# Kernel optimization log

Hardware: AMD Instinct MI355X
Metric: run time of the kernel (lower is better)

Reference implementation:

```python
import jax, jax.numpy as jnp
import numpy as np

B, L, S, V = 1024, 512, 64, 160000
EMB = 16
E = 3 * EMB            # extended embedding dim = 48
G, M = 4, 3            # lsh_group_num, lsh_group_length
MAXC = 2 ** M          # 8 buckets per group
NH, KD = 8, 4          # MHA heads / key_dim
IN_DIM = 5 * EMB + 3 * E   # user(80) + item(48) + longterm(48) + shortterm(48) = 224
PAD_LT, PAD_ST = L // 4, S // 4
M_VALUES = jnp.array([1, 2, 4], dtype=jnp.float32)
LN_EPS = 1e-3  # keras LayerNormalization default


def setup_inputs() -> dict:
    key = jax.random.key(0)
    ks = list(jax.random.split(key, 40))
    d = {}
    for i, n in enumerate(['uid', 'utag1', 'utag2', 'utag3', 'utag4']):
        d[n] = jax.random.randint(ks[i], (B,), 1, V, dtype=jnp.int32)
    for i, n in enumerate(['label_goods_ids', 'label_shop_ids', 'label_cate_ids']):
        d[n] = jax.random.randint(ks[5 + i], (B,), 1, V, dtype=jnp.int32)
    for i, n in enumerate(['longterm_goods_ids', 'longterm_shop_ids', 'longterm_cate_ids']):
        ids = jax.random.randint(ks[8 + i], (B, L), 1, V, dtype=jnp.int32)
        d[n] = ids.at[:, L - PAD_LT:].set(0)  # left-aligned valid prefix, padded tail
    for i, n in enumerate(['shortterm_goods_ids', 'shortterm_shop_ids', 'shortterm_cate_ids']):
        ids = jax.random.randint(ks[11 + i], (B, S), 1, V, dtype=jnp.int32)
        d[n] = ids.at[:, S - PAD_ST:].set(0)
    def nrm(k, shape, s):
        return jax.random.normal(k, shape, jnp.float32) * s
    d['embed_table'] = nrm(ks[14], (V, EMB), 0.05)
    d['H'] = nrm(ks[15], (E, G, M), 1.0)  # non-trainable LSH projections
    d['wq'] = nrm(ks[16], (E, NH, KD), 0.1); d['bq'] = jnp.zeros((NH, KD))
    d['wk'] = nrm(ks[17], (E, NH, KD), 0.1); d['bk'] = jnp.zeros((NH, KD))
    d['wv'] = nrm(ks[18], (E, NH, KD), 0.1); d['bv'] = jnp.zeros((NH, KD))
    d['wo'] = nrm(ks[19], (NH, KD, E), 0.1); d['bo'] = jnp.zeros((E,))
    d['w1'] = nrm(ks[20], (IN_DIM, 200), 0.1); d['b1'] = jnp.zeros((200,))
    d['g1'] = jnp.ones((200,)); d['be1'] = jnp.zeros((200,))
    d['w2'] = nrm(ks[21], (200, 80), 0.1); d['b2'] = jnp.zeros((80,))
    d['g2'] = jnp.ones((80,)); d['be2'] = jnp.zeros((80,))
    d['w3'] = nrm(ks[22], (80, 1), 0.1); d['b3'] = jnp.zeros((1,))
    return d


def _stack_embed(table, feats):
    # feats: list of (B,) or (B,T) int arrays -> (B, T, n_feats*EMB)
    cols = [f[:, None] if f.ndim == 1 else f for f in feats]
    X = jnp.stack(cols, axis=2)              # (B, T, F)
    Xe = table[X]                            # (B, T, F, EMB)
    return Xe.reshape(Xe.shape[0], Xe.shape[1], -1)


def _layernorm(x, g, b):
    mu = x.mean(-1, keepdims=True)
    var = jnp.square(x - mu).mean(-1, keepdims=True)
    return g * (x - mu) / jnp.sqrt(var + LN_EPS) + b


def _lsh_codes(x, H):
    # x: (B, T, E) -> integer bucket codes (B, T, G)
    codes = jnp.sign(jnp.einsum('bte,egm->btgm', x, H))
    binary = (codes == 1).astype(jnp.float32)
    return jnp.tensordot(binary, M_VALUES, axes=[[-1], [0]]).astype(jnp.int32)


def _forward(uid, utag1, utag2, utag3, utag4,
             label_goods_ids, label_shop_ids, label_cate_ids,
             longterm_goods_ids, longterm_shop_ids, longterm_cate_ids,
             shortterm_goods_ids, shortterm_shop_ids, shortterm_cate_ids,
             embed_table, H, wq, bq, wk, bk, wv, bv, wo, bo,
             w1, b1, g1, be1, w2, b2, g2, be2, w3, b3):
    # --- embeddings ---
    Xu = _stack_embed(embed_table, [uid, utag1, utag2, utag3, utag4])        # (B,1,80)
    Xi = _stack_embed(embed_table, [label_goods_ids, label_shop_ids, label_cate_ids])  # (B,1,48)
    Xl = _stack_embed(embed_table, [longterm_goods_ids, longterm_shop_ids, longterm_cate_ids])   # (B,L,48)
    Xs = _stack_embed(embed_table, [shortterm_goods_ids, shortterm_shop_ids, shortterm_cate_ids])  # (B,S,48)

    longterm_pad = longterm_goods_ids == 0
    shortterm_pad = shortterm_goods_ids == 0

    # --- long-term interest: LSH scatter-mean over buckets then gather by item code ---
    series_int = _lsh_codes(Xl, H)                                   # (B,L,G)
    mXl = Xl * (~longterm_pad).astype(jnp.float32)[:, :, None]        # masked series embeddings
    oh = jax.nn.one_hot(series_int, MAXC, dtype=jnp.float32)          # (B,L,G,C)
    c_sum = jnp.einsum('blgc,ble->bgce', oh, mXl)                     # bucket sums (B,G,C,E)
    vc = oh.sum(axis=1)                                               # valid counts (B,G,C)
    safe = jnp.where(vc[..., None] > 0,
                     c_sum / jnp.maximum(vc[..., None], 1.0),
                     0.0)                                             # bucket means
    item_int = _lsh_codes(Xi, H)                                      # (B,1,G)
    item_oh = jax.nn.one_hot(item_int, MAXC, dtype=jnp.float32)       # (B,1,G,C)
    longterm_interest = jnp.einsum('bgce,bsgc->bsge', safe, item_oh).mean(axis=2)  # (B,1,E)

    # --- short-term interest: target attention (keras MultiHeadAttention) ---
    lengths = (~shortterm_pad).astype(jnp.int32).sum(axis=1)           # (B,)
    seq_mask = (jnp.arange(S)[None, :] < lengths[:, None]).astype(jnp.float32)  # (B,S)
    q = jnp.einsum('bqe,ehd->bqhd', Xi, wq) + bq
    k = jnp.einsum('bke,ehd->bkhd', Xs, wk) + bk
    v = jnp.einsum('bke,ehd->bkhd', Xs, wv) + bv
    scores = jnp.einsum('bqhd,bkhd->bhqk', q, k) / jnp.sqrt(jnp.float32(KD))
    scores = scores + (1.0 - seq_mask[:, None, None, :]) * (-1e9)
    attn = jax.nn.softmax(scores, axis=-1)
    ctx = jnp.einsum('bhqk,bkhd->bqhd', attn, v)
    shortterm_interest = jnp.einsum('bqhd,hde->bqe', ctx, wo) + bo      # (B,1,E)

    # --- final MLP: Dense->LN->ReLU x2, Dense->sigmoid ---
    feat = jnp.concatenate([Xu[:, 0], Xi[:, 0],
                            longterm_interest[:, 0], shortterm_interest[:, 0]], axis=-1)  # (B,224)
    h = jax.nn.relu(_layernorm(feat @ w1 + b1, g1, be1))
    h = jax.nn.relu(_layernorm(h @ w2 + b2, g2, be2))
    return jax.nn.sigmoid(h @ w3 + b3)                                 # (B,1)


def reference(uid, utag1, utag2, utag3, utag4,
              label_goods_ids, label_shop_ids, label_cate_ids,
              longterm_goods_ids, longterm_shop_ids, longterm_cate_ids,
              shortterm_goods_ids, shortterm_shop_ids, shortterm_cate_ids,
              embed_table, H, wq, bq, wk, bk, wv, bv, wo, bo,
              w1, b1, g1, be1, w2, b2, g2, be2, w3, b3):
    return _forward(uid, utag1, utag2, utag3, utag4,
                    label_goods_ids, label_shop_ids, label_cate_ids,
                    longterm_goods_ids, longterm_shop_ids, longterm_cate_ids,
                    shortterm_goods_ids, shortterm_shop_ids, shortterm_cate_ids,
                    embed_table, H, wq, bq, wk, bk, wv, bv, wo, bo,
                    w1, b1, g1, be1, w2, b2, g2, be2, w3, b3)
```

## Files before the change

kernel.cpp:

```cpp
#include <hip/hip_runtime.h>
#include <hip/hip_bf16.h>

#define LLEN 512
#define SLEN 64
#define EMBD 16
#define EE 48
#define GG 4
#define NHH 8
#define KDD 4
#define INDIM 224
#define H1D 200
#define H2D 80
#define CHUNK 128
#define PXE 52
#define NT 512

__device__ __forceinline__ float bf2f(unsigned short u) {
    union { unsigned int i; float f; } v; v.i = ((unsigned int)u) << 16; return v.f;
}

template<bool BF16>
__device__ __forceinline__ float ldf(const void* p, int i) {
    if constexpr (BF16) return bf2f(((const unsigned short*)p)[i]);
    else                return ((const float*)p)[i];
}

template<bool BF16>
__device__ __forceinline__ float4 ld4(const void* p, int i4) {
    if constexpr (BF16) {
        ushort4 u = ((const ushort4*)p)[i4 >> 2];
        return make_float4(bf2f(u.x), bf2f(u.y), bf2f(u.z), bf2f(u.w));
    } else {
        return ((const float4*)p)[i4 >> 2];
    }
}

struct Pool {
    float buf[CHUNK * PXE + 16];
    float part[8][GG][EE];
    float hf[12 * EE];
    float feat[INDIM];
    float q[NHH * KDD];
    float red[128];
    int   pcw[8][2];
    int   icode[GG];
    int   len;
    float mu, rstd;
};

template<bool BF16>
__device__ void sdim_body(Pool& P,
    const int* uid, const int* ut1, const int* ut2, const int* ut3, const int* ut4,
    const int* lb_g, const int* lb_s, const int* lb_c,
    const int* lt_g, const int* lt_s, const int* lt_c,
    const int* st_g, const int* st_s, const int* st_c,
    const void* tbl, const void* Hm,
    const void* wq, const void* bq, const void* wk, const void* bk,
    const void* wvv, const void* bv, const void* wo, const void* bo,
    const void* w1, const void* b1, const void* g1, const void* be1,
    const void* w2, const void* b2, const void* g2, const void* be2,
    const void* w3, const void* b3, void* outp)
{
    const int b = blockIdx.x;
    const int tid = threadIdx.x;
    const int lane = tid & 63;
    const int wid = __builtin_amdgcn_readfirstlane(tid >> 6);

    for (int i = tid; i < 12 * EE; i += NT) {
        int j = i / EE, e = i - j * EE;
        P.hf[i] = ldf<BF16>(Hm, e * 12 + j);
    }
    if (tid < 80) {
        int f = tid >> 4, e = tid & 15;
        int id = (f == 0) ? uid[b] : (f == 1) ? ut1[b] : (f == 2) ? ut2[b] : (f == 3) ? ut3[b] : ut4[b];
        P.feat[tid] = ldf<BF16>(tbl, id * EMBD + e);
    } else if (tid < 128) {
        int t = tid - 80; int f = t >> 4, e = t & 15;
        int id = (f == 0) ? lb_g[b] : (f == 1) ? lb_s[b] : lb_c[b];
        P.feat[80 + t] = ldf<BF16>(tbl, id * EMBD + e);
    }
    __syncthreads();

    if (tid < 32) {
        float acc = ldf<BF16>(bq, tid);
        for (int e = 0; e < EE; e++) acc += P.feat[80 + e] * ldf<BF16>(wq, e * 32 + tid);
        P.q[tid] = acc;
    }
    if (tid >= 64 && tid < 76) {
        int j = tid - 64;
        float acc = 0.f;
        for (int e = 0; e < EE; e++) acc += P.feat[80 + e] * P.hf[j * EE + e];
        P.red[j] = acc;
    }
    __syncthreads();
    if (tid < GG) {
        int code = 0;
        #pragma unroll
        for (int m = 0; m < 3; m++) if (P.red[tid * 3 + m] > 0.f) code |= (1 << m);
        P.icode[tid] = code;
    }

    float accg[GG] = {0.f, 0.f, 0.f, 0.f};
    int cnt0 = 0, cnt1 = 0;
    const int offs = (lane < 52) ? lane : 51;
    const int pB = ((wid & 3) << 5) | (lane & 31);
    const int gB = ((wid >> 2) << 1) | (lane >> 5);

    for (int ch = 0; ch < LLEN / CHUNK; ch++) {
        const int base = ch * CHUNK;
        {
            int ids[3];
            #pragma unroll
            for (int i = 0; i < 3; i++) {
                int f = tid + NT * i;
                int p = f / 12, qq = f - 12 * p, fe = qq >> 2;
                const int* idp = (fe == 0) ? lt_g : (fe == 1) ? lt_s : lt_c;
                ids[i] = idp[b * LLEN + base + p];
            }
            float4 vs[3];
            #pragma unroll
            for (int i = 0; i < 3; i++) {
                int f = tid + NT * i;
                int p = f / 12, qq = f - 12 * p;
                vs[i] = ld4<BF16>(tbl, ids[i] * EMBD + ((qq & 3) << 2));
            }
            #pragma unroll
            for (int i = 0; i < 3; i++) {
                int f = tid + NT * i;
                int p = f / 12, qq = f - 12 * p;
                *(float4*)&P.buf[p * PXE + (qq << 2)] = vs[i];
            }
        }
        __syncthreads();
        {
            const float* row = &P.buf[pB * PXE];
            float4 x[12];
            #pragma unroll
            for (int k = 0; k < 12; k++) x[k] = *(const float4*)(row + 4 * k);
            float acc[3];
            #pragma unroll
            for (int jj = 0; jj < 3; jj++) {
                const float4* hr = (const float4*)&P.hf[(3 * gB + jj) * EE];
                float s = 0.f;
                #pragma unroll
                for (int k = 0; k < 12; k++) {
                    float4 h4 = hr[k];
                    s += x[k].x * h4.x + x[k].y * h4.y + x[k].z * h4.z + x[k].w * h4.w;
                }
                acc[jj] = s;
            }
            int code = 0;
            #pragma unroll
            for (int m = 0; m < 3; m++) if (acc[m] > 0.f) code |= (1 << m);
            int valid = (lt_g[b * LLEN + base + pB] != 0);
            P.buf[pB * PXE + 48 + gB] = (code == P.icode[gB] && valid) ? 1.f : 0.f;
            unsigned long long m = __ballot(code == P.icode[gB]);
            cnt0 += __popcll(m & 0xFFFFFFFFull);
            cnt1 += __popcll(m >> 32);
        }
        __syncthreads();
        {
            const float* basep = &P.buf[(wid << 4) * PXE] + offs;
            #pragma unroll
            for (int i = 0; i < 16; i++) {
                float xv = basep[i * PXE];
                #pragma unroll
                for (int g = 0; g < GG; g++) {
                    float sel = __int_as_float(
                        __builtin_amdgcn_readlane(__float_as_int(xv), 48 + g));
                    accg[g] += sel * xv;
                }
            }
        }
        __syncthreads();
    }
    if (lane < EE) {
        #pragma unroll
        for (int g = 0; g < GG; g++) P.part[wid][g][lane] = accg[g];
    }
    if (lane == 0) { P.pcw[wid][0] = cnt0; P.pcw[wid][1] = cnt1; }
    __syncthreads();

    if (tid < EE) {
        float r = 0.f;
        #pragma unroll
        for (int g = 0; g < GG; g++) {
            int wb = (g >> 1) << 2;
            int h = g & 1;
            float c = (float)(P.pcw[wb][h] + P.pcw[wb + 1][h] + P.pcw[wb + 2][h] + P.pcw[wb + 3][h]);
            float s = 0.f;
            #pragma unroll
            for (int w = 0; w < 8; w++) s += P.part[w][g][tid];
            r += s / fmaxf(c, 1.0f);
        }
        P.feat[128 + tid] = r * 0.25f;
    }

    float* Xs   = P.buf;
    float* wkq  = P.buf + SLEN * PXE;
    float* bkq  = wkq + EE * NHH;
    float* sc   = bkq + NHH;
    float* su   = sc + NHH * SLEN;
    float* sctx = su + NHH * EE;

    {
        int f0 = tid;
        int p0 = f0 / 12, q0 = f0 - 12 * p0, fe0 = q0 >> 2;
        const int* idp0 = (fe0 == 0) ? st_g : (fe0 == 1) ? st_s : st_c;
        int id0 = idp0[b * SLEN + p0];
        int id1 = 0, p1 = 0, q1 = 0;
        bool has1 = (tid < (SLEN * 12 - NT));
        if (has1) {
            int f1 = tid + NT;
            p1 = f1 / 12; q1 = f1 - 12 * p1; int fe1 = q1 >> 2;
            const int* idp1 = (fe1 == 0) ? st_g : (fe1 == 1) ? st_s : st_c;
            id1 = idp1[b * SLEN + p1];
        }
        float4 v0 = ld4<BF16>(tbl, id0 * EMBD + ((q0 & 3) << 2));
        *(float4*)&Xs[p0 * PXE + (q0 << 2)] = v0;
        if (has1) {
            float4 v1 = ld4<BF16>(tbl, id1 * EMBD + ((q1 & 3) << 2));
            *(float4*)&Xs[p1 * PXE + (q1 << 2)] = v1;
        }
    }
    if (tid < 64) {
        unsigned long long msk = __ballot(st_g[b * SLEN + tid] != 0);
        if (tid == 0) P.len = __popcll(msk);
    }
    for (int t = tid; t < EE * NHH; t += NT) {
        int e = t >> 3, h = t & 7;
        float acc = 0.f;
        #pragma unroll
        for (int d = 0; d < KDD; d++) acc += ldf<BF16>(wk, e * 32 + h * 4 + d) * P.q[h * 4 + d];
        wkq[t] = acc;
    }
    if (tid < NHH) {
        float acc = 0.f;
        #pragma unroll
        for (int d = 0; d < KDD; d++) acc += ldf<BF16>(bk, tid * 4 + d) * P.q[tid * 4 + d];
        bkq[tid] = acc;
    }
    __syncthreads();
    {
        int s = tid >> 3, h = tid & 7;
        float acc = bkq[h];
        for (int e = 0; e < EE; e++) acc += Xs[s * PXE + e] * wkq[e * NHH + h];
        acc *= 0.5f;
        if (s >= P.len) acc -= 1e9f;
        sc[s * NHH + h] = acc;
    }
    __syncthreads();
    {
        float v = sc[lane * NHH + wid];
        float mx = v;
        #pragma unroll
        for (int o = 32; o; o >>= 1) mx = fmaxf(mx, __shfl_xor(mx, o));
        float ex = __expf(v - mx);
        float sm = ex;
        #pragma unroll
        for (int o = 32; o; o >>= 1) sm += __shfl_xor(sm, o);
        sc[lane * NHH + wid] = ex / sm;
    }
    __syncthreads();
    if (tid < NHH * EE) {
        int h = tid / EE, e = tid - h * EE;
        float acc = 0.f;
        for (int s = 0; s < SLEN; s++) acc += sc[s * NHH + h] * Xs[s * PXE + e];
        su[tid] = acc;
    }
    __syncthreads();
    if (tid < 32) {
        float acc = ldf<BF16>(bv, tid);
        int h = tid >> 2;
        for (int e = 0; e < EE; e++) acc += su[h * EE + e] * ldf<BF16>(wvv, e * 32 + tid);
        sctx[tid] = acc;
    }
    __syncthreads();
    if (tid < EE) {
        float acc = ldf<BF16>(bo, tid);
        #pragma unroll
        for (int i = 0; i < 32; i++) acc += sctx[i] * ldf<BF16>(wo, i * EE + tid);
        P.feat[176 + tid] = acc;
    }
    __syncthreads();

    float z1p = 0.f;
    if (tid < H1D) {
        z1p = ldf<BF16>(b1, tid);
        for (int i = 0; i < 112; i++) z1p += P.feat[i] * ldf<BF16>(w1, i * H1D + tid);
    } else if (tid >= 256 && tid < 256 + H1D) {
        int o = tid - 256;
        float a = 0.f;
        for (int i = 112; i < INDIM; i++) a += P.feat[i] * ldf<BF16>(w1, i * H1D + o);
        P.buf[640 + o] = a;
    }
    __syncthreads();
    float z1 = 0.f;
    if (tid < H1D) { z1 = z1p + P.buf[640 + tid]; P.buf[tid] = z1; }
    __syncthreads();
    if (tid < 64) {
        float sm = 0.f, sq = 0.f;
        for (int j = tid; j < H1D; j += 64) { float v = P.buf[j]; sm += v; sq += v * v; }
        #pragma unroll
        for (int o = 32; o; o >>= 1) { sm += __shfl_xor(sm, o); sq += __shfl_xor(sq, o); }
        if (tid == 0) { float mu = sm / H1D; P.mu = mu; P.rstd = rsqrtf(sq / H1D - mu * mu + 1e-3f); }
    }
    __syncthreads();
    if (tid < H1D) {
        float h = fmaxf(ldf<BF16>(g1, tid) * (z1 - P.mu) * P.rstd + ldf<BF16>(be1, tid), 0.f);
        P.buf[256 + tid] = h;
    }
    __syncthreads();
    float z2p = 0.f;
    if (tid < H2D) {
        z2p = ldf<BF16>(b2, tid);
        for (int i = 0; i < 100; i++) z2p += P.buf[256 + i] * ldf<BF16>(w2, i * H2D + tid);
    } else if (tid >= 256 && tid < 256 + H2D) {
        int o = tid - 256;
        float a = 0.f;
        for (int i = 100; i < H1D; i++) a += P.buf[256 + i] * ldf<BF16>(w2, i * H2D + o);
        P.buf[640 + o] = a;
    }
    __syncthreads();
    float z2 = 0.f;
    if (tid < H2D) { z2 = z2p + P.buf[640 + tid]; P.buf[tid] = z2; }
    __syncthreads();
    if (tid < 64) {
        float sm = 0.f, sq = 0.f;
        for (int j = tid; j < H2D; j += 64) { float v = P.buf[j]; sm += v; sq += v * v; }
        #pragma unroll
        for (int o = 32; o; o >>= 1) { sm += __shfl_xor(sm, o); sq += __shfl_xor(sq, o); }
        if (tid == 0) { float mu = sm / H2D; P.mu = mu; P.rstd = rsqrtf(sq / H2D - mu * mu + 1e-3f); }
    }
    __syncthreads();
    if (tid < H2D) {
        float h = fmaxf(ldf<BF16>(g2, tid) * (z2 - P.mu) * P.rstd + ldf<BF16>(be2, tid), 0.f);
        P.red[tid] = h * ldf<BF16>(w3, tid);
    }
    __syncthreads();
    if (tid < 64) {
        float v = P.red[tid] + ((tid < H2D - 64) ? P.red[64 + tid] : 0.f);
        #pragma unroll
        for (int o = 32; o; o >>= 1) v += __shfl_xor(v, o);
        if (tid == 0) {
            float acc = ldf<BF16>(b3, 0) + v;
            float sig = 1.f / (1.f + __expf(-acc));
            if constexpr (BF16) ((__hip_bfloat16*)outp)[b] = __float2bfloat16(sig);
            else                ((float*)outp)[b] = sig;
        }
    }
}

__global__ __launch_bounds__(NT, 8) void sdim_fwd(
    const int* __restrict__ uid, const int* __restrict__ ut1, const int* __restrict__ ut2,
    const int* __restrict__ ut3, const int* __restrict__ ut4,
    const int* __restrict__ lb_g, const int* __restrict__ lb_s, const int* __restrict__ lb_c,
    const int* __restrict__ lt_g, const int* __restrict__ lt_s, const int* __restrict__ lt_c,
    const int* __restrict__ st_g, const int* __restrict__ st_s, const int* __restrict__ st_c,
    const void* __restrict__ tbl, const void* __restrict__ Hm,
    const void* __restrict__ wq, const void* __restrict__ bq,
    const void* __restrict__ wk, const void* __restrict__ bk,
    const void* __restrict__ wvv, const void* __restrict__ bv,
    const void* __restrict__ wo, const void* __restrict__ bo,
    const void* __restrict__ w1, const void* __restrict__ b1,
    const void* __restrict__ g1, const void* __restrict__ be1,
    const void* __restrict__ w2, const void* __restrict__ b2,
    const void* __restrict__ g2, const void* __restrict__ be2,
    const void* __restrict__ w3, const void* __restrict__ b3,
    void* __restrict__ outp)
{
    __shared__ Pool P;
    __shared__ int s_isbf;
    if (threadIdx.x < 64) {
        int big = 0;
        for (int i = (threadIdx.x & 63); i < 128; i += 64) {
            unsigned short u = ((const unsigned short*)tbl)[2 * i];
            if (((u >> 7) & 0xFF) >= 127) big = 1;
        }
        unsigned long long m = __ballot(big);
        if (threadIdx.x == 0) s_isbf = (m == 0ull) ? 1 : 0;
    }
    __syncthreads();
    if (s_isbf)
        sdim_body<true >(P, uid, ut1, ut2, ut3, ut4, lb_g, lb_s, lb_c, lt_g, lt_s, lt_c,
                         st_g, st_s, st_c, tbl, Hm, wq, bq, wk, bk, wvv, bv, wo, bo,
                         w1, b1, g1, be1, w2, b2, g2, be2, w3, b3, outp);
    else
        sdim_body<false>(P, uid, ut1, ut2, ut3, ut4, lb_g, lb_s, lb_c, lt_g, lt_s, lt_c,
                         st_g, st_s, st_c, tbl, Hm, wq, bq, wk, bk, wvv, bv, wo, bo,
                         w1, b1, g1, be1, w2, b2, g2, be2, w3, b3, outp);
}

extern "C" void kernel_launch(void* const* d_in, const int* in_sizes, int n_in,
                              void* d_out, int out_size, void* d_ws, size_t ws_size,
                              hipStream_t stream) {
    const int B = in_sizes[0];
    sdim_fwd<<<B, NT, 0, stream>>>(
        (const int*)d_in[0],  (const int*)d_in[1],  (const int*)d_in[2],
        (const int*)d_in[3],  (const int*)d_in[4],
        (const int*)d_in[5],  (const int*)d_in[6],  (const int*)d_in[7],
        (const int*)d_in[8],  (const int*)d_in[9],  (const int*)d_in[10],
        (const int*)d_in[11], (const int*)d_in[12], (const int*)d_in[13],
        (const void*)d_in[14], (const void*)d_in[15],
        (const void*)d_in[16], (const void*)d_in[17],
        (const void*)d_in[18], (const void*)d_in[19],
        (const void*)d_in[20], (const void*)d_in[21],
        (const void*)d_in[22], (const void*)d_in[23],
        (const void*)d_in[24], (const void*)d_in[25],
        (const void*)d_in[26], (const void*)d_in[27],
        (const void*)d_in[28], (const void*)d_in[29],
        (const void*)d_in[30], (const void*)d_in[31],
        (const void*)d_in[32], (const void*)d_in[33],
        d_out);
}
```

Before: 199.3 us.

## Software-pipeline embedding gathers across chunks and vectorize attention and MLP dot products

Prefetches the next chunk's long-term embedding rows into registers while the current chunk's LSH hashing and aggregation run. The short-term sequence gather is folded into the last iteration, and the query code is computed per thread instead of through shared memory. It also transposes the key-query weights for float4 score dot products and splits the MLP matmuls into four independent accumulators with float4 feature loads. These changes aim to hide global gather latency and cut serial FMA chains, at the cost of more registers and less occupancy.

```diff
diff --git a/kernel.cpp b/kernel.cpp
--- a/kernel.cpp
+++ b/kernel.cpp
@@ -25,15 +25,12 @@
     else                return ((const float*)p)[i];
 }
 
-template<bool BF16>
-__device__ __forceinline__ float4 ld4(const void* p, int i4) {
-    if constexpr (BF16) {
-        ushort4 u = ((const ushort4*)p)[i4 >> 2];
-        return make_float4(bf2f(u.x), bf2f(u.y), bf2f(u.z), bf2f(u.w));
-    } else {
-        return ((const float4*)p)[i4 >> 2];
-    }
-}
+template<bool BF16> struct RawSel { using T = float4; };
+template<>          struct RawSel<true> { using T = ushort4; };
+__device__ __forceinline__ float4 cvt4(ushort4 u) {
+    return make_float4(bf2f(u.x), bf2f(u.y), bf2f(u.z), bf2f(u.w));
+}
+__device__ __forceinline__ float4 cvt4(float4 f) { return f; }
 
 struct Pool {
     float buf[CHUNK * PXE + 16];
@@ -43,7 +40,6 @@
     float q[NHH * KDD];
     float red[128];
     int   pcw[8][2];
-    int   icode[GG];
     int   len;
     float mu, rstd;
 };
@@ -61,10 +57,29 @@
     const void* w2, const void* b2, const void* g2, const void* be2,
     const void* w3, const void* b3, void* outp)
 {
+    using RawT = typename RawSel<BF16>::T;
     const int b = blockIdx.x;
     const int tid = threadIdx.x;
     const int lane = tid & 63;
     const int wid = __builtin_amdgcn_readfirstlane(tid >> 6);
+
+    const int* jsrc[3]; int jq4[3], jlds[3];
+    #pragma unroll
+    for (int i = 0; i < 3; i++) {
+        int f = tid + NT * i;
+        int p = f / 12, qq = f - 12 * p, fe = qq >> 2;
+        const int* idp = (fe == 0) ? lt_g : (fe == 1) ? lt_s : lt_c;
+        jsrc[i] = idp + b * LLEN + p;
+        jq4[i]  = (qq & 3) << 2;
+        jlds[i] = p * PXE + (qq << 2);
+    }
+    const int pB = ((wid & 3) << 5) | (lane & 31);
+    const int gB = ((wid >> 2) << 1) | (lane >> 5);
+    const int* vsrc = lt_g + b * LLEN + pB;
+
+    int ids[3];
+    #pragma unroll
+    for (int i = 0; i < 3; i++) ids[i] = jsrc[i][0];
 
     for (int i = tid; i < 12 * EE; i += NT) {
         int j = i / EE, e = i - j * EE;
@@ -92,46 +107,44 @@
         for (int e = 0; e < EE; e++) acc += P.feat[80 + e] * P.hf[j * EE + e];
         P.red[j] = acc;
     }
-    __syncthreads();
-    if (tid < GG) {
-        int code = 0;
-        #pragma unroll
-        for (int m = 0; m < 3; m++) if (P.red[tid * 3 + m] > 0.f) code |= (1 << m);
-        P.icode[tid] = code;
-    }
+    {
+        RawT rv[3];
+        #pragma unroll
+        for (int i = 0; i < 3; i++) rv[i] = ((const RawT*)tbl)[(ids[i] * EMBD + jq4[i]) >> 2];
+        #pragma unroll
+        for (int i = 0; i < 3; i++) *(float4*)&P.buf[jlds[i]] = cvt4(rv[i]);
+    }
+    #pragma unroll
+    for (int i = 0; i < 3; i++) ids[i] = jsrc[i][CHUNK];
+    int vld = vsrc[0];
+    __syncthreads();
+
+    int icb = 0;
+    #pragma unroll
+    for (int m = 0; m < 3; m++) if (P.red[gB * 3 + m] > 0.f) icb |= (1 << m);
 
     float accg[GG] = {0.f, 0.f, 0.f, 0.f};
     int cnt0 = 0, cnt1 = 0;
     const int offs = (lane < 52) ? lane : 51;
-    const int pB = ((wid & 3) << 5) | (lane & 31);
-    const int gB = ((wid >> 2) << 1) | (lane >> 5);
-
-    for (int ch = 0; ch < LLEN / CHUNK; ch++) {
-        const int base = ch * CHUNK;
-        {
-            int ids[3];
-            #pragma unroll
-            for (int i = 0; i < 3; i++) {
-                int f = tid + NT * i;
-                int p = f / 12, qq = f - 12 * p, fe = qq >> 2;
-                const int* idp = (fe == 0) ? lt_g : (fe == 1) ? lt_s : lt_c;
-                ids[i] = idp[b * LLEN + base + p];
+    const bool has1 = (tid < (SLEN * 12 - NT));
+
+    for (int ch = 0; ch < 4; ++ch) {
+        RawT rvn[3];
+        int aid0 = 0, aid1 = 0, aq0 = 0, aq1 = 0, al0 = 0, al1 = 0;
+        if (ch < 3) {
+            #pragma unroll
+            for (int i = 0; i < 3; i++)
+                rvn[i] = ((const RawT*)tbl)[(ids[i] * EMBD + jq4[i]) >> 2];
+        } else {
+            int f0 = tid; int p0 = f0 / 12, q0 = f0 - 12 * p0, fe0 = q0 >> 2;
+            const int* idp0 = (fe0 == 0) ? st_g : (fe0 == 1) ? st_s : st_c;
+            aid0 = idp0[b * SLEN + p0]; aq0 = (q0 & 3) << 2; al0 = p0 * PXE + (q0 << 2);
+            if (has1) {
+                int f1 = tid + NT; int p1 = f1 / 12, q1 = f1 - 12 * p1, fe1 = q1 >> 2;
+                const int* idp1 = (fe1 == 0) ? st_g : (fe1 == 1) ? st_s : st_c;
+                aid1 = idp1[b * SLEN + p1]; aq1 = (q1 & 3) << 2; al1 = p1 * PXE + (q1 << 2);
             }
-            float4 vs[3];
-            #pragma unroll
-            for (int i = 0; i < 3; i++) {
-                int f = tid + NT * i;
-                int p = f / 12, qq = f - 12 * p;
-                vs[i] = ld4<BF16>(tbl, ids[i] * EMBD + ((qq & 3) << 2));
-            }
-            #pragma unroll
-            for (int i = 0; i < 3; i++) {
-                int f = tid + NT * i;
-                int p = f / 12, qq = f - 12 * p;
-                *(float4*)&P.buf[p * PXE + (qq << 2)] = vs[i];
-            }
-        }
-        __syncthreads();
+        }
         {
             const float* row = &P.buf[pB * PXE];
             float4 x[12];
@@ -152,9 +165,9 @@
             int code = 0;
             #pragma unroll
             for (int m = 0; m < 3; m++) if (acc[m] > 0.f) code |= (1 << m);
-            int valid = (lt_g[b * LLEN + base + pB] != 0);
-            P.buf[pB * PXE + 48 + gB] = (code == P.icode[gB] && valid) ? 1.f : 0.f;
-            unsigned long long m = __ballot(code == P.icode[gB]);
+            int valid = (vld != 0);
+            P.buf[pB * PXE + 48 + gB] = (code == icb && valid) ? 1.f : 0.f;
+            unsigned long long m = __ballot(code == icb);
             cnt0 += __popcll(m & 0xFFFFFFFFull);
             cnt1 += __popcll(m >> 32);
         }
@@ -172,13 +185,56 @@
                 }
             }
         }
+        RawT arv0, arv1;
+        if (ch == 3) {
+            arv0 = ((const RawT*)tbl)[(aid0 * EMBD + aq0) >> 2];
+            if (has1) arv1 = ((const RawT*)tbl)[(aid1 * EMBD + aq1) >> 2];
+        }
         __syncthreads();
-    }
+        if (ch < 3) {
+            #pragma unroll
+            for (int i = 0; i < 3; i++) *(float4*)&P.buf[jlds[i]] = cvt4(rvn[i]);
+            if (ch < 2) {
+                #pragma unroll
+                for (int i = 0; i < 3; i++) ids[i] = jsrc[i][(ch + 2) * CHUNK];
+            }
+            vld = vsrc[(ch + 1) * CHUNK];
+            __syncthreads();
+        } else {
+            *(float4*)&P.buf[al0] = cvt4(arv0);
+            if (has1) *(float4*)&P.buf[al1] = cvt4(arv1);
+        }
+    }
+
+    float* Xs   = P.buf;
+    float* wkqT = P.buf + SLEN * PXE;
+    float* bkq  = wkqT + NHH * PXE;
+    float* sc   = bkq + NHH;
+    float* su   = sc + SLEN * NHH;
+    float* sctx = su + NHH * EE;
+
     if (lane < EE) {
         #pragma unroll
         for (int g = 0; g < GG; g++) P.part[wid][g][lane] = accg[g];
     }
     if (lane == 0) { P.pcw[wid][0] = cnt0; P.pcw[wid][1] = cnt1; }
+    for (int t = tid; t < EE * NHH; t += NT) {
+        int e = t >> 3, h = t & 7;
+        float acc = 0.f;
+        #pragma unroll
+        for (int d = 0; d < KDD; d++) acc += ldf<BF16>(wk, e * 32 + h * 4 + d) * P.q[h * 4 + d];
+        wkqT[h * PXE + e] = acc;
+    }
+    if (tid < NHH) {
+        float acc = 0.f;
+        #pragma unroll
+        for (int d = 0; d < KDD; d++) acc += ldf<BF16>(bk, tid * 4 + d) * P.q[tid * 4 + d];
+        bkq[tid] = acc;
+    }
+    if (tid < 64) {
+        unsigned long long msk = __ballot(st_g[b * SLEN + tid] != 0);
+        if (tid == 0) P.len = __popcll(msk);
+    }
     __syncthreads();
 
     if (tid < EE) {
@@ -196,55 +252,17 @@
         P.feat[128 + tid] = r * 0.25f;
     }
 
-    float* Xs   = P.buf;
-    float* wkq  = P.buf + SLEN * PXE;
-    float* bkq  = wkq + EE * NHH;
-    float* sc   = bkq + NHH;
-    float* su   = sc + NHH * SLEN;
-    float* sctx = su + NHH * EE;
-
-    {
-        int f0 = tid;
-        int p0 = f0 / 12, q0 = f0 - 12 * p0, fe0 = q0 >> 2;
-        const int* idp0 = (fe0 == 0) ? st_g : (fe0 == 1) ? st_s : st_c;
-        int id0 = idp0[b * SLEN + p0];
-        int id1 = 0, p1 = 0, q1 = 0;
-        bool has1 = (tid < (SLEN * 12 - NT));
-        if (has1) {
-            int f1 = tid + NT;
-            p1 = f1 / 12; q1 = f1 - 12 * p1; int fe1 = q1 >> 2;
-            const int* idp1 = (fe1 == 0) ? st_g : (fe1 == 1) ? st_s : st_c;
-            id1 = idp1[b * SLEN + p1];
-        }
-        float4 v0 = ld4<BF16>(tbl, id0 * EMBD + ((q0 & 3) << 2));
-        *(float4*)&Xs[p0 * PXE + (q0 << 2)] = v0;
-        if (has1) {
-            float4 v1 = ld4<BF16>(tbl, id1 * EMBD + ((q1 & 3) << 2));
-            *(float4*)&Xs[p1 * PXE + (q1 << 2)] = v1;
-        }
-    }
-    if (tid < 64) {
-        unsigned long long msk = __ballot(st_g[b * SLEN + tid] != 0);
-        if (tid == 0) P.len = __popcll(msk);
-    }
-    for (int t = tid; t < EE * NHH; t += NT) {
-        int e = t >> 3, h = t & 7;
-        float acc = 0.f;
-        #pragma unroll
-        for (int d = 0; d < KDD; d++) acc += ldf<BF16>(wk, e * 32 + h * 4 + d) * P.q[h * 4 + d];
-        wkq[t] = acc;
-    }
-    if (tid < NHH) {
-        float acc = 0.f;
-        #pragma unroll
-        for (int d = 0; d < KDD; d++) acc += ldf<BF16>(bk, tid * 4 + d) * P.q[tid * 4 + d];
-        bkq[tid] = acc;
-    }
-    __syncthreads();
     {
         int s = tid >> 3, h = tid & 7;
+        const float* xr = &Xs[s * PXE];
+        const float* wr = &wkqT[h * PXE];
         float acc = bkq[h];
-        for (int e = 0; e < EE; e++) acc += Xs[s * PXE + e] * wkq[e * NHH + h];
+        #pragma unroll
+        for (int k = 0; k < 12; k++) {
+            float4 xv = *(const float4*)(xr + 4 * k);
+            float4 wv = *(const float4*)(wr + 4 * k);
+            acc += xv.x * wv.x + xv.y * wv.y + xv.z * wv.z + xv.w * wv.w;
+        }
         acc *= 0.5f;
         if (s >= P.len) acc -= 1e9f;
         sc[s * NHH + h] = acc;
@@ -265,6 +283,7 @@
     if (tid < NHH * EE) {
         int h = tid / EE, e = tid - h * EE;
         float acc = 0.f;
+        #pragma unroll 4
         for (int s = 0; s < SLEN; s++) acc += sc[s * NHH + h] * Xs[s * PXE + e];
         su[tid] = acc;
     }
@@ -286,13 +305,28 @@
 
     float z1p = 0.f;
     if (tid < H1D) {
-        z1p = ldf<BF16>(b1, tid);
-        for (int i = 0; i < 112; i++) z1p += P.feat[i] * ldf<BF16>(w1, i * H1D + tid);
+        float a0 = ldf<BF16>(b1, tid), a1 = 0.f, a2 = 0.f, a3 = 0.f;
+        #pragma unroll 2
+        for (int i = 0; i < 112; i += 4) {
+            float4 f4 = *(const float4*)&P.feat[i];
+            a0 += f4.x * ldf<BF16>(w1, (i + 0) * H1D + tid);
+            a1 += f4.y * ldf<BF16>(w1, (i + 1) * H1D + tid);
+            a2 += f4.z * ldf<BF16>(w1, (i + 2) * H1D + tid);
+            a3 += f4.w * ldf<BF16>(w1, (i + 3) * H1D + tid);
+        }
+        z1p = (a0 + a1) + (a2 + a3);
     } else if (tid >= 256 && tid < 256 + H1D) {
         int o = tid - 256;
-        float a = 0.f;
-        for (int i = 112; i < INDIM; i++) a += P.feat[i] * ldf<BF16>(w1, i * H1D + o);
-        P.buf[640 + o] = a;
+        float a0 = 0.f, a1 = 0.f, a2 = 0.f, a3 = 0.f;
+        #pragma unroll 2
+        for (int i = 112; i < INDIM; i += 4) {
+            float4 f4 = *(const float4*)&P.feat[i];
+            a0 += f4.x * ldf<BF16>(w1, (i + 0) * H1D + o);
+            a1 += f4.y * ldf<BF16>(w1, (i + 1) * H1D + o);
+            a2 += f4.z * ldf<BF16>(w1, (i + 2) * H1D + o);
+            a3 += f4.w * ldf<BF16>(w1, (i + 3) * H1D + o);
+        }
+        P.buf[640 + o] = (a0 + a1) + (a2 + a3);
     }
     __syncthreads();
     float z1 = 0.f;
@@ -313,13 +347,28 @@
     __syncthreads();
     float z2p = 0.f;
     if (tid < H2D) {
-        z2p = ldf<BF16>(b2, tid);
-        for (int i = 0; i < 100; i++) z2p += P.buf[256 + i] * ldf<BF16>(w2, i * H2D + tid);
+        float a0 = ldf<BF16>(b2, tid), a1 = 0.f, a2 = 0.f, a3 = 0.f;
+        #pragma unroll 2
+        for (int i = 0; i < 100; i += 4) {
+            float4 f4 = *(const float4*)&P.buf[256 + i];
+            a0 += f4.x * ldf<BF16>(w2, (i + 0) * H2D + tid);
+            a1 += f4.y * ldf<BF16>(w2, (i + 1) * H2D + tid);
+            a2 += f4.z * ldf<BF16>(w2, (i + 2) * H2D + tid);
+            a3 += f4.w * ldf<BF16>(w2, (i + 3) * H2D + tid);
+        }
+        z2p = (a0 + a1) + (a2 + a3);
     } else if (tid >= 256 && tid < 256 + H2D) {
         int o = tid - 256;
-        float a = 0.f;
-        for (int i = 100; i < H1D; i++) a += P.buf[256 + i] * ldf<BF16>(w2, i * H2D + o);
-        P.buf[640 + o] = a;
+        float a0 = 0.f, a1 = 0.f, a2 = 0.f, a3 = 0.f;
+        #pragma unroll 2
+        for (int i = 100; i < H1D; i += 4) {
+            float4 f4 = *(const float4*)&P.buf[256 + i];
+            a0 += f4.x * ldf<BF16>(w2, (i + 0) * H2D + o);
+            a1 += f4.y * ldf<BF16>(w2, (i + 1) * H2D + o);
+            a2 += f4.z * ldf<BF16>(w2, (i + 2) * H2D + o);
+            a3 += f4.w * ldf<BF16>(w2, (i + 3) * H2D + o);
+        }
+        P.buf[640 + o] = (a0 + a1) + (a2 + a3);
     }
     __syncthreads();
     float z2 = 0.f;
```

Measured after the change: 236.8 us. 18.8% more time.
